# Kernel tuning notes

Hardware: AMD Instinct MI355X
Metric: run time of the kernel (lower is better)

The kernel has to match this reference:

```python
import jax, jax.numpy as jnp
import numpy as np

MAX_BITS = 8   # codes are stored at 8 bits (max of supported_bits), 4 codes per int32
W_BITS = 4     # active bit-width -> lut has 2**W_BITS entries per output row


def setup_inputs() -> dict:
    key = jax.random.key(0)
    k1, k2, k3 = jax.random.split(key, 3)
    B, S = 1, 2048
    OUT, IN = 8192, 8192
    x = jax.random.normal(k1, (B, S, IN), dtype=jnp.float32)
    qweight = jax.random.randint(k2, (OUT, IN // 4), 0, 2147483647, dtype=jnp.int32)
    # per-output-channel lookup table for w_bits=4 -> 16 entries
    lut = jax.random.normal(k3, (OUT, 2 ** W_BITS), dtype=jnp.float32)
    return {"x": x, "qweight": qweight, "lut": lut}


def dequant_kbit(qweight, lut, w_bits):
    # qweight: (O, K//4) int32 -> 8-bit codes (O, K)
    O = qweight.shape[0]
    shifts = jnp.array([0, 8, 16, 24], dtype=jnp.int32)
    codes = (qweight[:, :, None] >> shifts) & 0xFF          # (O, K//4, 4)
    codes = codes.reshape(O, -1)                             # (O, K)
    # any-precision: top w_bits of the 8-bit code index the w_bits LUT
    idx = codes >> (MAX_BITS - w_bits)                       # (O, K) in [0, 2**w_bits)
    weight = jnp.take_along_axis(lut, idx, axis=1)           # (O, K)
    return weight


def reference(x, qweight, lut):
    # bulk path of AnyprecisionLinear.forward (tokens > 8): dequant then matmul
    weight = dequant_kbit(qweight, lut, W_BITS)              # (O, K)
    out = jnp.einsum('bsk,ok->bso', x, weight)               # (B, S, O)
    return out
```

## Files before the change

### kernel.cpp

```cpp
#include <hip/hip_runtime.h>
#include <stdint.h>


#define M_DIM 2048
#define N_DIM 8192
#define K_DIM 8192
#define BM 128
#define BN 128
#define BK 64

typedef __bf16 bf16x8 __attribute__((ext_vector_type(8)));
typedef float f32x4 __attribute__((ext_vector_type(4)));

__device__ __forceinline__ unsigned int f2bf(float f) {
  unsigned int u = __float_as_uint(f);
  return (u + 0x7FFFu + ((u >> 16) & 1u)) >> 16;
}

__global__ __launch_bounds__(256) void dequant_kernel(
    const int4* __restrict__ qw4,
    const float* __restrict__ lut,
    unsigned short* __restrict__ wb) {
  __shared__ unsigned short slut[64 * 34];
  const int row = blockIdx.x;
  const int tid = threadIdx.x;

  for (int t = tid; t < 64 * 16; t += 256) {
    int c = t >> 4, e = t & 15;
    slut[c * 34 + e] = (unsigned short)f2bf(lut[row * 16 + e]);
  }
  __syncthreads();

  const unsigned short* myl = slut + (tid & 63) * 34;
  const int4* src = qw4 + (size_t)row * 512;
  unsigned short* dst = wb + (size_t)row * (size_t)K_DIM;

#pragma unroll
  for (int h = 0; h < 2; ++h) {
    const int i4 = h * 256 + tid;
    int4 q = src[i4];
    unsigned int w[4] = {(unsigned int)q.x, (unsigned int)q.y,
                         (unsigned int)q.z, (unsigned int)q.w};
    unsigned int v[16];
#pragma unroll
    for (int j = 0; j < 4; ++j) {
#pragma unroll
      for (int k = 0; k < 4; ++k) {
        v[j * 4 + k] = myl[(w[j] >> (8 * k + 4)) & 15u];
      }
    }
    uint4 o0, o1;
    o0.x = v[0] | (v[1] << 16);  o0.y = v[2]  | (v[3] << 16);
    o0.z = v[4] | (v[5] << 16);  o0.w = v[6]  | (v[7] << 16);
    o1.x = v[8] | (v[9] << 16);  o1.y = v[10] | (v[11] << 16);
    o1.z = v[12] | (v[13] << 16); o1.w = v[14] | (v[15] << 16);
    uint4* dp = (uint4*)(dst + (size_t)i4 * 16);
    dp[0] = o0;
    dp[1] = o1;
  }
}

__global__ __launch_bounds__(256) void cvt_x_kernel(
    const float4* __restrict__ x4, unsigned int* __restrict__ xb) {
  const int idx = blockIdx.x * 256 + threadIdx.x;
  float4 a = x4[2 * idx];
  float4 b = x4[2 * idx + 1];
  uint4 o;
  o.x = f2bf(a.x) | (f2bf(a.y) << 16);
  o.y = f2bf(a.z) | (f2bf(a.w) << 16);
  o.z = f2bf(b.x) | (f2bf(b.y) << 16);
  o.w = f2bf(b.z) | (f2bf(b.w) << 16);
  ((uint4*)xb)[idx] = o;
}

__global__ __launch_bounds__(256) void gemm_bt(
    const unsigned short* __restrict__ A,
    const unsigned short* __restrict__ B,
    float* __restrict__ C) {
  __shared__ __align__(16) unsigned short sA[BM * BK];
  __shared__ __align__(16) unsigned short sB[BN * BK];

  const int tid = threadIdx.x;
  const int wave = tid >> 6;
  const int lane = tid & 63;
  const int m0 = blockIdx.y * BM;
  const int n0 = blockIdx.x * BN;
  const int wm = (wave & 1) * 64;
  const int wn = (wave >> 1) * 64;

  const int srow = lane >> 3;
  const int scol = ((lane & 7) ^ (lane >> 3)) * 8;

  const int laneM = lane & 15;
  const int q = lane >> 4;
  const int sw = laneM & 7;

  f32x4 acc[4][4];
#pragma unroll
  for (int i = 0; i < 4; ++i)
#pragma unroll
    for (int j = 0; j < 4; ++j)
      acc[i][j] = (f32x4){0.0f, 0.0f, 0.0f, 0.0f};

  for (int k0 = 0; k0 < K_DIM; k0 += BK) {
#pragma unroll
    for (int r = 0; r < 4; ++r) {
      const int chunk = wave * 4 + r;
      const int row = chunk * 8 + srow;
      const unsigned short* ga = A + (size_t)(m0 + row) * K_DIM + k0 + scol;
      __builtin_amdgcn_global_load_lds(
          (const __attribute__((address_space(1))) void*)ga,
          (__attribute__((address_space(3))) void*)(sA + chunk * 512),
          16, 0, 0);
      const unsigned short* gb = B + (size_t)(n0 + row) * K_DIM + k0 + scol;
      __builtin_amdgcn_global_load_lds(
          (const __attribute__((address_space(1))) void*)gb,
          (__attribute__((address_space(3))) void*)(sB + chunk * 512),
          16, 0, 0);
    }
    __syncthreads();

#pragma unroll
    for (int kk = 0; kk < BK; kk += 32) {
      bf16x8 af[4], bfr[4];
#pragma unroll
      for (int t = 0; t < 4; ++t) {
        const int ra = wm + t * 16 + laneM;
        const int rb = wn + t * 16 + laneM;
        const int c = ((kk >> 3) + q) ^ sw;
        af[t]  = *(const bf16x8*)(sA + ra * BK + c * 8);
        bfr[t] = *(const bf16x8*)(sB + rb * BK + c * 8);
      }
#pragma unroll
      for (int i = 0; i < 4; ++i)
#pragma unroll
        for (int j = 0; j < 4; ++j)
          acc[i][j] = __builtin_amdgcn_mfma_f32_16x16x32_bf16(
              af[i], bfr[j], acc[i][j], 0, 0, 0);
    }
    __syncthreads();
  }

  const int crow = wm + (q << 2);
  const int ccol = wn + laneM;
#pragma unroll
  for (int i = 0; i < 4; ++i)
#pragma unroll
    for (int j = 0; j < 4; ++j) {
      float* cp = C + (size_t)(m0 + crow + i * 16) * N_DIM + (n0 + ccol + j * 16);
#pragma unroll
      for (int r2 = 0; r2 < 4; ++r2)
        cp[(size_t)r2 * N_DIM] = acc[i][j][r2];
    }
}

__global__ void naive_kernel(const float* __restrict__ x,
                             const int* __restrict__ qw,
                             const float* __restrict__ lut,
                             float* __restrict__ out) {
  int o = blockIdx.x * blockDim.x + threadIdx.x;
  int s = blockIdx.y;
  const float* xr = x + (size_t)s * K_DIM;
  const unsigned int* qr = (const unsigned int*)qw + (size_t)o * (K_DIM / 4);
  const float* l = lut + o * 16;
  float acc = 0.f;
  for (int w = 0; w < K_DIM / 4; ++w) {
    unsigned int q = qr[w];
    acc += xr[w * 4 + 0] * l[(q >> 4) & 15u]
         + xr[w * 4 + 1] * l[(q >> 12) & 15u]
         + xr[w * 4 + 2] * l[(q >> 20) & 15u]
         + xr[w * 4 + 3] * l[(q >> 28) & 15u];
  }
  out[(size_t)s * N_DIM + o] = acc;
}

extern "C" void kernel_launch(void* const* d_in, const int* in_sizes, int n_in,
                              void* d_out, int out_size, void* d_ws, size_t ws_size,
                              hipStream_t stream) {
  const float* x   = (const float*)d_in[0];
  const int*   qw  = (const int*)d_in[1];
  const float* lut = (const float*)d_in[2];
  float* out = (float*)d_out;

  const size_t wb_elems = (size_t)N_DIM * K_DIM;
  const size_t xb_elems = (size_t)M_DIM * K_DIM;
  const size_t need = (wb_elems + xb_elems) * sizeof(unsigned short);

  if (ws_size >= need) {
    unsigned short* wb = (unsigned short*)d_ws;
    unsigned short* xb = wb + wb_elems;

    hipLaunchKernelGGL(dequant_kernel, dim3(N_DIM), dim3(256), 0, stream,
                       (const int4*)qw, lut, wb);

    const int n_thr = M_DIM * K_DIM / 8;
    hipLaunchKernelGGL(cvt_x_kernel, dim3(n_thr / 256), dim3(256), 0, stream,
                       (const float4*)x, (unsigned int*)xb);

    dim3 grid(N_DIM / BN, M_DIM / BM);
    hipLaunchKernelGGL(gemm_bt, grid, dim3(256), 0, stream, xb, wb, out);
  } else {
    dim3 grid(N_DIM / 256, M_DIM);
    hipLaunchKernelGGL(naive_kernel, grid, dim3(256), 0, stream, x, qw, lut, out);
  }
}
```

Before: 532.5 us.

## Switch GEMM to 32x32x16 MFMA and restructure dequant LUT per wave

The GEMM inner loop moves from 16x16x32 bf16 MFMA tiles to 32x32x16 tiles, with each wave holding 2x2 accumulators of 16 floats. This cuts LDS fragment loads per MFMA and uses the larger instruction shape, with matching changes to the fragment indexing and output store mapping. The dequant kernel now handles four rows per block, one per wave, and keeps a per-lane transposed bf16 LUT in shared memory so lookups avoid bank conflicts and block-wide syncs. The 32x32 output layout writes 16 strided rows per lane, which may change store coalescing.

After: 498.7 us. 1.07x faster.

```diff
diff --git a/kernel.cpp b/kernel.cpp
--- a/kernel.cpp
+++ b/kernel.cpp
@@ -10,7 +10,7 @@
 #define BK 64
 
 typedef __bf16 bf16x8 __attribute__((ext_vector_type(8)));
-typedef float f32x4 __attribute__((ext_vector_type(4)));
+typedef float f32x16 __attribute__((ext_vector_type(16)));
 
 __device__ __forceinline__ unsigned int f2bf(float f) {
   unsigned int u = __float_as_uint(f);
@@ -21,40 +21,37 @@
     const int4* __restrict__ qw4,
     const float* __restrict__ lut,
     unsigned short* __restrict__ wb) {
-  __shared__ unsigned short slut[64 * 34];
-  const int row = blockIdx.x;
-  const int tid = threadIdx.x;
-
-  for (int t = tid; t < 64 * 16; t += 256) {
-    int c = t >> 4, e = t & 15;
-    slut[c * 34 + e] = (unsigned short)f2bf(lut[row * 16 + e]);
-  }
-  __syncthreads();
-
-  const unsigned short* myl = slut + (tid & 63) * 34;
-  const int4* src = qw4 + (size_t)row * 512;
-  unsigned short* dst = wb + (size_t)row * (size_t)K_DIM;
-
-#pragma unroll
-  for (int h = 0; h < 2; ++h) {
-    const int i4 = h * 256 + tid;
-    int4 q = src[i4];
+  __shared__ unsigned int slut[4 * 16 * 64];
+  const int wave = threadIdx.x >> 6;
+  const int lane = threadIdx.x & 63;
+  const int row = (blockIdx.x << 2) + wave;
+
+  unsigned int* tbl = slut + wave * (16 * 64) + lane;
+  const float* lr = lut + row * 16;
+#pragma unroll
+  for (int e = 0; e < 16; ++e) tbl[e * 64] = f2bf(lr[e]);
+
+  const int4* src = qw4 + (size_t)row * 512 + lane;
+  unsigned short* dst = wb + (size_t)row * K_DIM + lane * 16;
+
+#pragma unroll
+  for (int it = 0; it < 8; ++it) {
+    int4 q = src[it * 64];
     unsigned int w[4] = {(unsigned int)q.x, (unsigned int)q.y,
                          (unsigned int)q.z, (unsigned int)q.w};
     unsigned int v[16];
 #pragma unroll
     for (int j = 0; j < 4; ++j) {
 #pragma unroll
-      for (int k = 0; k < 4; ++k) {
-        v[j * 4 + k] = myl[(w[j] >> (8 * k + 4)) & 15u];
-      }
+      for (int k = 0; k < 4; ++k)
+        v[j * 4 + k] = tbl[((w[j] >> (8 * k + 4)) & 15u) * 64];
     }
     uint4 o0, o1;
-    o0.x = v[0] | (v[1] << 16);  o0.y = v[2]  | (v[3] << 16);
-    o0.z = v[4] | (v[5] << 16);  o0.w = v[6]  | (v[7] << 16);
-    o1.x = v[8] | (v[9] << 16);  o1.y = v[10] | (v[11] << 16);
+    o0.x = v[0] | (v[1] << 16);   o0.y = v[2]  | (v[3] << 16);
+    o0.z = v[4] | (v[5] << 16);   o0.w = v[6]  | (v[7] << 16);
+    o1.x = v[8] | (v[9] << 16);   o1.y = v[10] | (v[11] << 16);
     o1.z = v[12] | (v[13] << 16); o1.w = v[14] | (v[15] << 16);
-    uint4* dp = (uint4*)(dst + (size_t)i4 * 16);
+    uint4* dp = (uint4*)(dst + it * 1024);
     dp[0] = o0;
     dp[1] = o1;
   }
@@ -91,16 +88,17 @@
   const int srow = lane >> 3;
   const int scol = ((lane & 7) ^ (lane >> 3)) * 8;
 
-  const int laneM = lane & 15;
-  const int q = lane >> 4;
-  const int sw = laneM & 7;
-
-  f32x4 acc[4][4];
-#pragma unroll
-  for (int i = 0; i < 4; ++i)
-#pragma unroll
-    for (int j = 0; j < 4; ++j)
-      acc[i][j] = (f32x4){0.0f, 0.0f, 0.0f, 0.0f};
+  const int laneN = lane & 31;
+  const int half = lane >> 5;
+  const int sw = laneN & 7;
+
+  f32x16 acc[2][2];
+#pragma unroll
+  for (int i = 0; i < 2; ++i)
+#pragma unroll
+    for (int j = 0; j < 2; ++j)
+#pragma unroll
+      for (int r = 0; r < 16; ++r) acc[i][j][r] = 0.0f;
 
   for (int k0 = 0; k0 < K_DIM; k0 += BK) {
 #pragma unroll
@@ -121,36 +119,35 @@
     __syncthreads();
 
 #pragma unroll
-    for (int kk = 0; kk < BK; kk += 32) {
-      bf16x8 af[4], bfr[4];
-#pragma unroll
-      for (int t = 0; t < 4; ++t) {
-        const int ra = wm + t * 16 + laneM;
-        const int rb = wn + t * 16 + laneM;
-        const int c = ((kk >> 3) + q) ^ sw;
-        af[t]  = *(const bf16x8*)(sA + ra * BK + c * 8);
-        bfr[t] = *(const bf16x8*)(sB + rb * BK + c * 8);
+    for (int kk = 0; kk < BK; kk += 16) {
+      const int c = ((kk >> 3) + half) ^ sw;
+      bf16x8 af[2], bfr[2];
+#pragma unroll
+      for (int t = 0; t < 2; ++t) {
+        af[t]  = *(const bf16x8*)(sA + (wm + t * 32 + laneN) * BK + c * 8);
+        bfr[t] = *(const bf16x8*)(sB + (wn + t * 32 + laneN) * BK + c * 8);
       }
 #pragma unroll
-      for (int i = 0; i < 4; ++i)
-#pragma unroll
-        for (int j = 0; j < 4; ++j)
-          acc[i][j] = __builtin_amdgcn_mfma_f32_16x16x32_bf16(
+      for (int i = 0; i < 2; ++i)
+#pragma unroll
+        for (int j = 0; j < 2; ++j)
+          acc[i][j] = __builtin_amdgcn_mfma_f32_32x32x16_bf16(
               af[i], bfr[j], acc[i][j], 0, 0, 0);
     }
     __syncthreads();
   }
 
-  const int crow = wm + (q << 2);
-  const int ccol = wn + laneM;
-#pragma unroll
-  for (int i = 0; i < 4; ++i)
-#pragma unroll
-    for (int j = 0; j < 4; ++j) {
-      float* cp = C + (size_t)(m0 + crow + i * 16) * N_DIM + (n0 + ccol + j * 16);
-#pragma unroll
-      for (int r2 = 0; r2 < 4; ++r2)
-        cp[(size_t)r2 * N_DIM] = acc[i][j][r2];
+#pragma unroll
+  for (int i = 0; i < 2; ++i)
+#pragma unroll
+    for (int j = 0; j < 2; ++j) {
+      const int rbase = m0 + wm + i * 32 + 4 * half;
+      const int col = n0 + wn + j * 32 + laneN;
+#pragma unroll
+      for (int r = 0; r < 16; ++r) {
+        const int rrow = rbase + (r & 3) + 8 * (r >> 2);
+        C[(size_t)rrow * N_DIM + col] = acc[i][j][r];
+      }
     }
 }
 
@@ -190,7 +187,7 @@
     unsigned short* wb = (unsigned short*)d_ws;
     unsigned short* xb = wb + wb_elems;
 
-    hipLaunchKernelGGL(dequant_kernel, dim3(N_DIM), dim3(256), 0, stream,
+    hipLaunchKernelGGL(dequant_kernel, dim3(N_DIM / 4), dim3(256), 0, stream,
                        (const int4*)qw, lut, wb);
 
     const int n_thr = M_DIM * K_DIM / 8;
```
